# Kernel optimization log

Hardware: AMD Instinct MI355X
Metric: run time of the kernel (lower is better)

The kernel has to match this reference:

```python
import jax, jax.numpy as jnp
import numpy as np

NUM_GRAPHS = 16
NODES_PER = 1024
D = 128
H = 2
KPOS = 20
E = 262144


def _ln(x, g, b):
    mu = jnp.mean(x, axis=-1, keepdims=True)
    var = jnp.mean((x - mu) ** 2, axis=-1, keepdims=True)
    return (x - mu) * jax.lax.rsqrt(var + 1e-5) * g + b


def setup_inputs() -> dict:
    key = jax.random.key(0)
    ks = jax.random.split(key, 12)
    N = NUM_GRAPHS * NODES_PER
    s = 0.02
    return {
        "x": jax.random.normal(ks[0], (N, D), jnp.float32),
        "pos_enc": jax.random.normal(ks[1], (N, KPOS), jnp.float32),
        "pe_w": jax.random.normal(ks[2], (D, KPOS), jnp.float32) * s,
        "pe_b": jnp.zeros((D,), jnp.float32),
        "in_w": jax.random.normal(ks[3], (3 * D, D), jnp.float32) * s,
        "in_b": jnp.zeros((3 * D,), jnp.float32),
        "out_w": jax.random.normal(ks[4], (D, D), jnp.float32) * s,
        "out_b": jnp.zeros((D,), jnp.float32),
        "ln1_g": jnp.ones((D,), jnp.float32),
        "ln1_b": jnp.zeros((D,), jnp.float32),
        "ln2_g": jnp.ones((D,), jnp.float32),
        "ln2_b": jnp.zeros((D,), jnp.float32),
        "ff1_w": jax.random.normal(ks[5], (4 * D, D), jnp.float32) * s,
        "ff1_b": jnp.zeros((4 * D,), jnp.float32),
        "ff2_w": jax.random.normal(ks[6], (D, 4 * D), jnp.float32) * s,
        "ff2_b": jnp.zeros((D,), jnp.float32),
        "edge_index": jax.random.randint(ks[7], (2, E), 0, N, dtype=jnp.int32),
        "batch": jnp.repeat(jnp.arange(NUM_GRAPHS, dtype=jnp.int32), NODES_PER),
    }


def reference(x, pos_enc, pe_w, pe_b, in_w, in_b, out_w, out_b,
              ln1_g, ln1_b, ln2_g, ln2_b, ff1_w, ff1_b, ff2_w, ff2_b,
              edge_index, batch):
    # pos_enc Linear + add, then per-graph transformer (graphs equal-sized -> batched)
    h = x + pos_enc @ pe_w.T + pe_b  # (N, D)
    h = h.reshape(NUM_GRAPHS, NODES_PER, D)  # (B, S, D)

    hd = D // H
    qkv = h @ in_w.T + in_b  # (B, S, 3D)
    q, k, v = jnp.split(qkv, 3, axis=-1)

    def heads(t):
        return t.reshape(NUM_GRAPHS, NODES_PER, H, hd).transpose(0, 2, 1, 3)

    q, k, v = heads(q), heads(k), heads(v)  # (B, H, S, hd)
    scores = jnp.einsum('bhqd,bhkd->bhqk', q, k) / jnp.float32(np.sqrt(hd))
    attn = jax.nn.softmax(scores, axis=-1)
    ctx = jnp.einsum('bhqk,bhkd->bhqd', attn, v)
    ctx = ctx.transpose(0, 2, 1, 3).reshape(NUM_GRAPHS, NODES_PER, D)
    sa = ctx @ out_w.T + out_b

    # post-norm (PyTorch TransformerEncoderLayer default, eval mode: no dropout)
    h = _ln(h + sa, ln1_g, ln1_b)
    ff = jax.nn.relu(h @ ff1_w.T + ff1_b) @ ff2_w.T + ff2_b
    h = _ln(h + ff, ln2_g, ln2_b)
    return h.reshape(-1, D)
```

## Files before the change

### kernel.cpp

```cpp
#include <hip/hip_runtime.h>

typedef unsigned short u16;

#define NGRAPH 16
#define SEQ    1024
#define DIM    128
#define NHEAD  2
#define HDIM   64
#define KPOS   20
#define NTOT   (NGRAPH*SEQ)
#define QKVD   (3*DIM)

__device__ __forceinline__ float bf2f(u16 u) {
    return __uint_as_float(((unsigned int)u) << 16);
}
__device__ __forceinline__ u16 f2bf(float f) {
    unsigned int u = __float_as_uint(f);
    u += 0x7fffu + ((u >> 16) & 1u);
    return (u16)(u >> 16);
}

template<int CTRL>
__device__ __forceinline__ float dpp_ror(float x) {
    return __int_as_float(__builtin_amdgcn_update_dpp(
        __float_as_int(x), __float_as_int(x), CTRL, 0xF, 0xF, true));
}
__device__ __forceinline__ float row16_max(float x) {
    x = fmaxf(x, dpp_ror<0x121>(x));
    x = fmaxf(x, dpp_ror<0x122>(x));
    x = fmaxf(x, dpp_ror<0x124>(x));
    x = fmaxf(x, dpp_ror<0x128>(x));
    return x;
}
__device__ __forceinline__ float row16_sum(float x) {
    x += dpp_ror<0x121>(x);
    x += dpp_ror<0x122>(x);
    x += dpp_ror<0x124>(x);
    x += dpp_ror<0x128>(x);
    return x;
}

__device__ __forceinline__ float ld1(const void* p, int fbf, size_t i) {
    return fbf ? bf2f(((const u16*)p)[i]) : ((const float*)p)[i];
}
__device__ __forceinline__ float4 ldw8(const void* W, int fbf, size_t i) {
    if (fbf) return *(const float4*)((const u16*)W + i);
    const float* q = (const float*)W + i;
    float4 a = *(const float4*)q, b = *(const float4*)(q + 4);
    float4 r;
    u16* d = (u16*)&r;
    d[0]=f2bf(a.x); d[1]=f2bf(a.y); d[2]=f2bf(a.z); d[3]=f2bf(a.w);
    d[4]=f2bf(b.x); d[5]=f2bf(b.y); d[6]=f2bf(b.z); d[7]=f2bf(b.w);
    return r;
}

typedef __attribute__((ext_vector_type(8))) short bf16x8;
typedef __attribute__((ext_vector_type(4))) float f32x4;

__device__ __forceinline__ void gload16(const u16* g, u16* l) {
    __builtin_amdgcn_global_load_lds(
        (const __attribute__((address_space(1))) unsigned int*)(g),
        (__attribute__((address_space(3))) unsigned int*)(l), 16, 0, 0);
}
#define VMCNT0() asm volatile("s_waitcnt vmcnt(0)" ::: "memory")

__device__ __forceinline__ int detect_bf16(const u16* x) {
    int ok = 1;
    for (int i = 0; i < 256; i += 2) {
        unsigned e = (x[i] >> 7) & 0xFF;
        if (e < 60u || e > 180u) ok = 0;
    }
    return ok;
}
__global__ void detect_kernel(const u16* __restrict__ x, int* __restrict__ flag) {
    if (threadIdx.x == 0 && blockIdx.x == 0) *flag = detect_bf16(x);
}

__global__ __launch_bounds__(256)
void wconv_kernel(const void* __restrict__ in_w, const void* __restrict__ out_w,
                  const void* __restrict__ ff1_w, const void* __restrict__ ff2_w,
                  const u16* __restrict__ x,
                  u16* __restrict__ wbf, int* __restrict__ flag) {
    __shared__ int fsh;
    if (threadIdx.x == 0) {
        int ok = detect_bf16(x);
        fsh = ok;
        if (blockIdx.x == 0) *flag = ok;
    }
    __syncthreads();
    int fbf = fsh;
    int i8 = (blockIdx.x * 256 + threadIdx.x) * 8;
    const void* src; int off;
    if      (i8 <  49152) { src = in_w;  off = i8; }
    else if (i8 <  65536) { src = out_w; off = i8 - 49152; }
    else if (i8 < 131072) { src = ff1_w; off = i8 - 65536; }
    else                  { src = ff2_w; off = i8 - 131072; }
    *(float4*)&wbf[i8] = ldw8(src, fbf, off);
}

__global__ __launch_bounds__(256)
void pe_kernel(const void* __restrict__ x, const void* __restrict__ pos,
               const void* __restrict__ pe_w, const void* __restrict__ pe_b,
               u16* __restrict__ h0, const int* __restrict__ flag) {
    int fbf = *flag;
    __shared__ float wsh[DIM][KPOS + 1];
    int t = threadIdx.x;
    for (int i = t; i < DIM * KPOS; i += 256)
        wsh[i / KPOS][i % KPOS] = ld1(pe_w, fbf, i);
    __syncthreads();
    int row = blockIdx.x * 2 + (t >> 7), d = t & 127;
    float acc = 0.f;
#pragma unroll
    for (int k = 0; k < KPOS; ++k)
        acc += ld1(pos, fbf, (size_t)row * KPOS + k) * wsh[d][k];
    int rs = fbf ? 128 : 256;
    h0[(size_t)row * rs + d] =
        f2bf(ld1(x, fbf, (size_t)row * DIM + d) + acc + ld1(pe_b, fbf, d));
}

__global__ __launch_bounds__(256)
void qkvpe_kernel(const void* __restrict__ x, const void* __restrict__ pos,
                  const void* __restrict__ pe_w, const void* __restrict__ pe_b,
                  const u16* __restrict__ W, const void* __restrict__ bias,
                  u16* __restrict__ h0, u16* __restrict__ qkv,
                  u16* __restrict__ vt, const int* __restrict__ flag) {
    int fbf = *flag;
    int rs  = fbf ? 128 : 256;
    __shared__ __align__(16) u16 Ash[64][128];
    __shared__ __align__(16) u16 Wsh[2][128][128];
    __shared__ float wsh[DIM][KPOS + 1];
    __shared__ float possh[64][KPOS + 1];
    int t = threadIdx.x;
    int w = t >> 6, lane = t & 63, l16 = lane & 15, quad = lane >> 4;
    int n0 = blockIdx.x * 64;
    int xr = (l16 & 7) << 3;

#pragma unroll
    for (int i = 0; i < 8; ++i) {
        int r = w * 4 + i * 16 + (lane >> 4);
        int s = (lane & 15) ^ (r & 7);
        gload16(&W[(size_t)r * 128 + s * 8], &Wsh[0][w * 4 + i * 16][0]);
    }
    for (int i = t; i < DIM * KPOS; i += 256)
        wsh[i / KPOS][i % KPOS] = ld1(pe_w, fbf, i);
    for (int i = t; i < 64 * KPOS; i += 256)
        possh[i / KPOS][i % KPOS] =
            ld1(pos, fbf, (size_t)(n0 + i / KPOS) * KPOS + i % KPOS);
    asm volatile("s_waitcnt lgkmcnt(0)" ::: "memory");
    __builtin_amdgcn_s_barrier();

#pragma unroll
    for (int u = 0; u < 4; ++u) {
        int gu = t + u * 256;
        int r = gu >> 4, g = gu & 15;
        float4 hv;
        u16* hp = (u16*)&hv;
#pragma unroll
        for (int j = 0; j < 8; ++j) {
            int d = g * 8 + j;
            float a = ld1(x, fbf, (size_t)(n0 + r) * DIM + d) + ld1(pe_b, fbf, d);
#pragma unroll
            for (int k = 0; k < KPOS; ++k) a += possh[r][k] * wsh[d][k];
            hp[j] = f2bf(a);
        }
        *(float4*)&Ash[r][(g ^ (r & 7)) * 8] = hv;
        *(float4*)&h0[(size_t)(n0 + r) * rs + g * 8] = hv;
    }
    asm volatile("s_waitcnt lgkmcnt(0)" ::: "memory");
    __builtin_amdgcn_s_barrier();

#pragma unroll
    for (int m = 0; m < 3; ++m) {
        int m0 = m * 128;
        if (m < 2) {
#pragma unroll
            for (int i = 0; i < 8; ++i) {
                int r = w * 4 + i * 16 + (lane >> 4);
                int s = (lane & 15) ^ (r & 7);
                gload16(&W[(size_t)(m0 + 128 + r) * 128 + s * 8],
                        &Wsh[(m + 1) & 1][w * 4 + i * 16][0]);
            }
            asm volatile("s_waitcnt vmcnt(8)" ::: "memory");
        } else {
            asm volatile("s_waitcnt vmcnt(0)" ::: "memory");
        }
        __builtin_amdgcn_s_barrier();
        f32x4 acc[8] = {};
        __builtin_amdgcn_s_setprio(1);
#pragma unroll
        for (int kk = 0; kk < 4; ++kk) {
            bf16x8 af = *(const bf16x8*)&Ash[w * 16 + l16][(kk * 32 + quad * 8) ^ xr];
#pragma unroll
            for (int s = 0; s < 8; ++s) {
                bf16x8 bf = *(const bf16x8*)&Wsh[m & 1][s * 16 + l16][(kk * 32 + quad * 8) ^ xr];
                acc[s] = __builtin_amdgcn_mfma_f32_16x16x32_bf16(af, bf, acc[s], 0, 0, 0);
            }
        }
        __builtin_amdgcn_s_setprio(0);
        float bb[8];
#pragma unroll
        for (int s = 0; s < 8; ++s) bb[s] = ld1(bias, fbf, m0 + s * 16 + l16);
#pragma unroll
        for (int r = 0; r < 4; ++r) {
            int lr = w * 16 + quad * 4 + r;
            if (m == 2) {
                int n = n0 + lr;
                int bg = n >> 10, nl = n & 1023;
#pragma unroll
                for (int s = 0; s < 8; ++s)
                    vt[((size_t)(bg * 128) + s * 16 + l16) * SEQ + nl] =
                        f2bf(acc[s][r] + bb[s]);
            } else {
#pragma unroll
                for (int s = 0; s < 8; ++s)
                    qkv[(size_t)(n0 + lr) * QKVD + m0 + s * 16 + l16] =
                        f2bf(acc[s][r] + bb[s]);
            }
        }
        if (m < 2) __builtin_amdgcn_s_barrier();
    }
}

__global__ __launch_bounds__(256)
void attnout_kernel(const u16* __restrict__ qkv, const u16* __restrict__ vtp,
                    const u16* __restrict__ Wout, const void* __restrict__ out_b,
                    const void* __restrict__ lng, const void* __restrict__ lnb,
                    u16* __restrict__ h01, const int* __restrict__ flag) {
    int fbf = *flag;
    int rs  = fbf ? 128 : 256;
    __shared__ __align__(16) u16 Qsh[64][72];
    __shared__ __align__(16) u16 Ksh[2][64][64];
    __shared__ __align__(16) u16 Vsh[2][64][64];
    __shared__ u16 Psh[64][72];
    __shared__ __align__(16) u16 CtxSh[64][128];
    __shared__ __align__(16) u16 Wsh[128][128];
    int t    = threadIdx.x;
    int w    = t >> 6;
    int lane = t & 63;
    int l16  = lane & 15;
    int quad = lane >> 4;
    int xr   = (l16 & 7) << 3;
    int L = blockIdx.x;
    int g8 = L & 7; int rest = L >> 3;
    int qt = rest & 15; int b = (rest >> 4) * 8 + g8;
    int n0 = b * SEQ + qt * 64;

#pragma unroll
    for (int i = 0; i < 8; ++i) {
        int r = w * 4 + i * 16 + (lane >> 4);
        int s = (lane & 15) ^ (r & 7);
        gload16(&Wout[(size_t)r * 128 + s * 8], &Wsh[w * 4 + i * 16][0]);
    }

#pragma unroll 1
    for (int h = 0; h < NHEAD; ++h) {
#pragma unroll
        for (int i = 0; i < 2; ++i) {
            int idx = t + i * 256;
            int r = idx >> 3, d8 = (idx & 7) * 8;
            float4 qv = *(const float4*)&qkv[(size_t)(n0 + r) * QKVD + h * HDIM + d8];
            u16* qp = (u16*)&qv;
#pragma unroll
            for (int j = 0; j < 8; ++j) qp[j] = f2bf(bf2f(qp[j]) * 0.125f);
            *(float4*)&Qsh[r][d8] = qv;
        }
        const u16* kbase = qkv + (size_t)b * SEQ * QKVD + DIM + h * HDIM;
        const u16* vbase = vtp + (size_t)((b * 2 + h) * 64) * SEQ;

        auto stageKV = [&](int kt, int bf2) {
#pragma unroll
            for (int i = 0; i < 2; ++i) {
                int r = w * 8 + i * 32 + (lane >> 3);
                int s = (lane & 7) ^ (r & 7);
                gload16(&kbase[(size_t)(kt * 64 + r) * QKVD + s * 8],
                        &Ksh[bf2][w * 8 + i * 32][0]);
            }
#pragma unroll
            for (int i = 0; i < 2; ++i) {
                int r = w * 8 + i * 32 + (lane >> 3);
                int s = (lane & 7) ^ (r & 7);
                gload16(&vbase[(size_t)r * SEQ + kt * 64 + s * 8],
                        &Vsh[bf2][w * 8 + i * 32][0]);
            }
        };

        stageKV(0, 0);
        VMCNT0();
        __syncthreads();
        bf16x8 qa0 = *(const bf16x8*)&Qsh[w * 16 + l16][quad * 8];
        bf16x8 qa1 = *(const bf16x8*)&Qsh[w * 16 + l16][32 + quad * 8];

        f32x4 o[4] = {};
        float mrow[4] = {-1e30f, -1e30f, -1e30f, -1e30f};
        float lrow[4] = {};

#pragma unroll 1
        for (int kt = 0; kt < SEQ / 64; ++kt) {
            int cur = kt & 1;
            if (kt + 1 < SEQ / 64) stageKV(kt + 1, cur ^ 1);

            float sc[4][4];
            __builtin_amdgcn_s_setprio(1);
#pragma unroll
            for (int c = 0; c < 4; ++c) {
                bf16x8 kb0 = *(const bf16x8*)&Ksh[cur][c * 16 + l16][(quad * 8) ^ xr];
                bf16x8 kb1 = *(const bf16x8*)&Ksh[cur][c * 16 + l16][(32 + quad * 8) ^ xr];
                f32x4 s = {};
                s = __builtin_amdgcn_mfma_f32_16x16x32_bf16(qa0, kb0, s, 0, 0, 0);
                s = __builtin_amdgcn_mfma_f32_16x16x32_bf16(qa1, kb1, s, 0, 0, 0);
#pragma unroll
                for (int r = 0; r < 4; ++r) sc[c][r] = s[r];
            }
            __builtin_amdgcn_s_setprio(0);
            float alpha[4];
#pragma unroll
            for (int r = 0; r < 4; ++r) {
                float mx = fmaxf(fmaxf(sc[0][r], sc[1][r]), fmaxf(sc[2][r], sc[3][r]));
                mx = row16_max(mx);
                float mnew = fmaxf(mrow[r], mx);
                alpha[r] = __expf(mrow[r] - mnew);
                mrow[r] = mnew;
                float sum = 0.f;
#pragma unroll
                for (int c = 0; c < 4; ++c) {
                    float p = __expf(sc[c][r] - mnew);
                    sc[c][r] = p;
                    sum += p;
                }
                sum = row16_sum(sum);
                lrow[r] = lrow[r] * alpha[r] + sum;
            }
#pragma unroll
            for (int c = 0; c < 4; ++c)
#pragma unroll
                for (int r = 0; r < 4; ++r)
                    Psh[w * 16 + quad * 4 + r][c * 16 + l16] = f2bf(sc[c][r]);
#pragma unroll
            for (int dt = 0; dt < 4; ++dt)
#pragma unroll
                for (int r = 0; r < 4; ++r) o[dt][r] *= alpha[r];
            bf16x8 pa0 = *(const bf16x8*)&Psh[w * 16 + l16][quad * 8];
            bf16x8 pa1 = *(const bf16x8*)&Psh[w * 16 + l16][32 + quad * 8];
            __builtin_amdgcn_s_setprio(1);
#pragma unroll
            for (int dt = 0; dt < 4; ++dt) {
                bf16x8 vb0 = *(const bf16x8*)&Vsh[cur][dt * 16 + l16][(quad * 8) ^ xr];
                bf16x8 vb1 = *(const bf16x8*)&Vsh[cur][dt * 16 + l16][(32 + quad * 8) ^ xr];
                o[dt] = __builtin_amdgcn_mfma_f32_16x16x32_bf16(pa0, vb0, o[dt], 0, 0, 0);
                o[dt] = __builtin_amdgcn_mfma_f32_16x16x32_bf16(pa1, vb1, o[dt], 0, 0, 0);
            }
            __builtin_amdgcn_s_setprio(0);
            if (kt + 1 < SEQ / 64) {
                VMCNT0();
                __syncthreads();
            }
        }
#pragma unroll
        for (int r = 0; r < 4; ++r) {
            float inv = 1.f / lrow[r];
            int lr = w * 16 + quad * 4 + r;
#pragma unroll
            for (int dt = 0; dt < 4; ++dt) {
                int e = h * HDIM + dt * 16 + l16;
                int g = e >> 3;
                CtxSh[lr][((g ^ (lr & 7)) << 3) + (e & 7)] =
                    f2bf(o[dt][r] * inv);
            }
        }
        __syncthreads();
    }

    VMCNT0();
    f32x4 acc[8] = {};
    __builtin_amdgcn_s_setprio(1);
#pragma unroll
    for (int kk = 0; kk < 4; ++kk) {
        bf16x8 af = *(const bf16x8*)&CtxSh[w * 16 + l16][(kk * 32 + quad * 8) ^ xr];
#pragma unroll
        for (int s = 0; s < 8; ++s) {
            bf16x8 bf = *(const bf16x8*)&Wsh[s * 16 + l16][(kk * 32 + quad * 8) ^ xr];
            acc[s] = __builtin_amdgcn_mfma_f32_16x16x32_bf16(af, bf, acc[s], 0, 0, 0);
        }
    }
    __builtin_amdgcn_s_setprio(0);
    float bb[8], gg[8], be[8];
#pragma unroll
    for (int s = 0; s < 8; ++s) {
        bb[s] = ld1(out_b, fbf, s * 16 + l16);
        gg[s] = ld1(lng, fbf, s * 16 + l16);
        be[s] = ld1(lnb, fbf, s * 16 + l16);
    }
#pragma unroll
    for (int r = 0; r < 4; ++r) {
        int lr = w * 16 + quad * 4 + r;
        size_t rg = (size_t)(n0 + lr);
        float v[8];
#pragma unroll
        for (int s = 0; s < 8; ++s)
            v[s] = acc[s][r] + bb[s] + bf2f(h01[rg * rs + s * 16 + l16]);
        float sm = 0.f, sq = 0.f;
#pragma unroll
        for (int s = 0; s < 8; ++s) { sm += v[s]; sq += v[s] * v[s]; }
        sm = row16_sum(sm);
        sq = row16_sum(sq);
        float mu  = sm * (1.f / DIM);
        float var = fmaxf(sq * (1.f / DIM) - mu * mu, 0.f);
        float rsq = rsqrtf(var + 1e-5f);
#pragma unroll
        for (int s = 0; s < 8; ++s)
            h01[rg * rs + s * 16 + l16] =
                f2bf((v[s] - mu) * rsq * gg[s] + be[s]);
    }
}

__global__ __launch_bounds__(256)
void ffn_kernel(const u16* __restrict__ h1, const u16* __restrict__ W1,
                const u16* __restrict__ W2, const void* __restrict__ b1,
                const void* __restrict__ b2,
                const void* __restrict__ lng, const void* __restrict__ lnb,
                void* __restrict__ outp, const int* __restrict__ flag) {
    int fbf = *flag;
    int rs  = fbf ? 128 : 256;
    __shared__ __align__(16) u16 Ash[64][128];
    __shared__ __align__(16) u16 Wsh[2][128][128];
    __shared__ __align__(16) u16 F1sh[4][64][128];
    int t = threadIdx.x;
    int w = t >> 6, lane = t & 63, l16 = lane & 15, quad = lane >> 4;
    int n0 = blockIdx.x * 64;
    int xr = (l16 & 7) << 3;

#pragma unroll
    for (int i = 0; i < 4; ++i) {
        int r = w * 4 + i * 16 + (lane >> 4);
        int s = (lane & 15) ^ (r & 7);
        gload16(&h1[(size_t)(n0 + r) * rs + s * 8], &Ash[w * 4 + i * 16][0]);
    }
#pragma unroll
    for (int i = 0; i < 8; ++i) {
        int r = w * 4 + i * 16 + (lane >> 4);
        int s = (lane & 15) ^ (r & 7);
        gload16(&W1[(size_t)r * 128 + s * 8], &Wsh[0][w * 4 + i * 16][0]);
    }

#pragma unroll
    for (int m = 0; m < 4; ++m) {
#pragma unroll
        for (int i = 0; i < 8; ++i) {
            int r = w * 4 + i * 16 + (lane >> 4);
            int s = (lane & 15) ^ (r & 7);
            if (m < 3)
                gload16(&W1[(size_t)((m + 1) * 128 + r) * 128 + s * 8],
                        &Wsh[(m + 1) & 1][w * 4 + i * 16][0]);
            else
                gload16(&W2[(size_t)r * 512 + s * 8],
                        &Wsh[0][w * 4 + i * 16][0]);
        }
        asm volatile("s_waitcnt vmcnt(8)" ::: "memory");
        __builtin_amdgcn_s_barrier();
        f32x4 acc[8] = {};
        __builtin_amdgcn_s_setprio(1);
#pragma unroll
        for (int kk = 0; kk < 4; ++kk) {
            bf16x8 af = *(const bf16x8*)&Ash[w * 16 + l16][(kk * 32 + quad * 8) ^ xr];
#pragma unroll
            for (int s = 0; s < 8; ++s) {
                bf16x8 bf = *(const bf16x8*)&Wsh[m & 1][s * 16 + l16][(kk * 32 + quad * 8) ^ xr];
                acc[s] = __builtin_amdgcn_mfma_f32_16x16x32_bf16(af, bf, acc[s], 0, 0, 0);
            }
        }
        __builtin_amdgcn_s_setprio(0);
        float bb[8];
#pragma unroll
        for (int s = 0; s < 8; ++s) bb[s] = ld1(b1, fbf, m * 128 + s * 16 + l16);
#pragma unroll
        for (int r = 0; r < 4; ++r) {
            int lr = w * 16 + quad * 4 + r;
#pragma unroll
            for (int s = 0; s < 8; ++s) {
                int g = s * 2 + (l16 >> 3);
                F1sh[m][lr][((g ^ (lr & 7)) << 3) + (l16 & 7)] =
                    f2bf(fmaxf(acc[s][r] + bb[s], 0.f));
            }
        }
        asm volatile("s_waitcnt lgkmcnt(0)" ::: "memory");
        __builtin_amdgcn_s_barrier();
    }

    f32x4 acc2[8] = {};
#pragma unroll
    for (int c = 0; c < 4; ++c) {
        if (c < 3) {
#pragma unroll
            for (int i = 0; i < 8; ++i) {
                int r = w * 4 + i * 16 + (lane >> 4);
                int s = (lane & 15) ^ (r & 7);
                gload16(&W2[(size_t)r * 512 + (c + 1) * 128 + s * 8],
                        &Wsh[(c + 1) & 1][w * 4 + i * 16][0]);
            }
            asm volatile("s_waitcnt vmcnt(8)" ::: "memory");
        } else {
            asm volatile("s_waitcnt vmcnt(0)" ::: "memory");
        }
        __builtin_amdgcn_s_barrier();
        __builtin_amdgcn_s_setprio(1);
#pragma unroll
        for (int kk = 0; kk < 4; ++kk) {
            bf16x8 af = *(const bf16x8*)&F1sh[c][w * 16 + l16][(kk * 32 + quad * 8) ^ xr];
#pragma unroll
            for (int s = 0; s < 8; ++s) {
                bf16x8 bf = *(const bf16x8*)&Wsh[c & 1][s * 16 + l16][(kk * 32 + quad * 8) ^ xr];
                acc2[s] = __builtin_amdgcn_mfma_f32_16x16x32_bf16(af, bf, acc2[s], 0, 0, 0);
            }
        }
        __builtin_amdgcn_s_setprio(0);
        if (c < 3) __builtin_amdgcn_s_barrier();
    }

    float bb[8], gg[8], be[8];
#pragma unroll
    for (int s = 0; s < 8; ++s) {
        bb[s] = ld1(b2, fbf, s * 16 + l16);
        gg[s] = ld1(lng, fbf, s * 16 + l16);
        be[s] = ld1(lnb, fbf, s * 16 + l16);
    }
#pragma unroll
    for (int r = 0; r < 4; ++r) {
        int lr = w * 16 + quad * 4 + r;
        size_t rg = (size_t)(n0 + lr);
        float v[8];
#pragma unroll
        for (int s = 0; s < 8; ++s) {
            int g = s * 2 + (l16 >> 3);
            float resid = bf2f(Ash[lr][((g ^ (lr & 7)) << 3) + (l16 & 7)]);
            v[s] = acc2[s][r] + bb[s] + resid;
        }
        float sm = 0.f, sq = 0.f;
#pragma unroll
        for (int s = 0; s < 8; ++s) { sm += v[s]; sq += v[s] * v[s]; }
        sm = row16_sum(sm);
        sq = row16_sum(sq);
        float mu  = sm * (1.f / DIM);
        float var = fmaxf(sq * (1.f / DIM) - mu * mu, 0.f);
        float rsq = rsqrtf(var + 1e-5f);
        if (fbf) {
            u16* o = (u16*)outp;
#pragma unroll
            for (int s = 0; s < 8; ++s)
                o[rg * 128 + s * 16 + l16] =
                    f2bf((v[s] - mu) * rsq * gg[s] + be[s]);
        } else {
            float* o = (float*)outp;
#pragma unroll
            for (int s = 0; s < 8; ++s)
                o[rg * 128 + s * 16 + l16] =
                    (v[s] - mu) * rsq * gg[s] + be[s];
        }
    }
}

template<int EPI, int NK>
__global__ __launch_bounds__(256)
void mgemm_kernel(const u16* __restrict__ A, const void* __restrict__ W,
                  int wbf16, const void* __restrict__ bias,
                  const u16* __restrict__ resid,
                  const void* __restrict__ lng, const void* __restrict__ lnb,
                  void* __restrict__ outp, u16* __restrict__ vt,
                  int Mtot, int AstrIn,
                  int arow0, int orow0, const int* __restrict__ flag) {
    const int K = NK * 128;
    int fbf  = *flag;
    int wfmt = wbf16 ? 1 : fbf;
    int rs   = fbf ? 128 : 256;
    int Astr = (AstrIn < 0) ? rs : AstrIn;
    __shared__ u16 Ash[64][136];
    __shared__ u16 Wsh[128][136];
    int t = threadIdx.x;
    int w = t >> 6, lane = t & 63, l16 = lane & 15, quad = lane >> 4;
    int n0 = blockIdx.x * 64;
    int m0 = blockIdx.y * 128;
    f32x4 acc[8] = {};
    float4 aR[4], wR[8];
#pragma unroll
    for (int i = 0; i < 4; ++i) {
        int idx = t + i * 256;
        int row = idx >> 4, k8 = (idx & 15) * 8;
        aR[i] = *(const float4*)&A[(size_t)(arow0 + n0 + row) * Astr + k8];
    }
#pragma unroll
    for (int i = 0; i < 8; ++i) {
        int idx = t + i * 256;
        int row = idx >> 4, k8 = (idx & 15) * 8;
        wR[i] = ldw8(W, wfmt, (size_t)(m0 + row) * K + k8);
    }
#pragma unroll 1
    for (int c = 0; c < NK; ++c) {
#pragma unroll
        for (int i = 0; i < 4; ++i) {
            int idx = t + i * 256;
            *(float4*)&Ash[idx >> 4][(idx & 15) * 8] = aR[i];
        }
#pragma unroll
        for (int i = 0; i < 8; ++i) {
            int idx = t + i * 256;
            *(float4*)&Wsh[idx >> 4][(idx & 15) * 8] = wR[i];
        }
        __syncthreads();
        if (c + 1 < NK) {
            int kc = (c + 1) * 128;
#pragma unroll
            for (int i = 0; i < 4; ++i) {
                int idx = t + i * 256;
                int row = idx >> 4, k8 = (idx & 15) * 8;
                aR[i] = *(const float4*)&A[(size_t)(arow0 + n0 + row) * Astr + kc + k8];
            }
#pragma unroll
            for (int i = 0; i < 8; ++i) {
                int idx = t + i * 256;
                int row = idx >> 4, k8 = (idx & 15) * 8;
                wR[i] = ldw8(W, wfmt, (size_t)(m0 + row) * K + kc + k8);
            }
        }
        __builtin_amdgcn_s_setprio(1);
#pragma unroll
        for (int kk = 0; kk < 4; ++kk) {
            bf16x8 af = *(const bf16x8*)&Ash[w * 16 + l16][kk * 32 + quad * 8];
#pragma unroll
            for (int s = 0; s < 8; ++s) {
                bf16x8 bf = *(const bf16x8*)&Wsh[s * 16 + l16][kk * 32 + quad * 8];
                acc[s] = __builtin_amdgcn_mfma_f32_16x16x32_bf16(af, bf, acc[s], 0, 0, 0);
            }
        }
        __builtin_amdgcn_s_setprio(0);
        if (c + 1 < NK) __syncthreads();
    }
    float bb[8];
#pragma unroll
    for (int s = 0; s < 8; ++s) bb[s] = ld1(bias, fbf, m0 + s * 16 + l16);
    float gg[8], be[8];
    if (EPI >= 2) {
#pragma unroll
        for (int s = 0; s < 8; ++s) {
            gg[s] = ld1(lng, fbf, s * 16 + l16);
            be[s] = ld1(lnb, fbf, s * 16 + l16);
        }
    }
#pragma unroll
    for (int r = 0; r < 4; ++r) {
        int lr = w * 16 + quad * 4 + r;
        float v[8];
#pragma unroll
        for (int s = 0; s < 8; ++s) {
            v[s] = acc[s][r] + bb[s];
            if (EPI == 1) v[s] = fmaxf(v[s], 0.f);
        }
        if (EPI <= 1) {
            u16* o = (u16*)outp;
#pragma unroll
            for (int s = 0; s < 8; ++s)
                o[(size_t)(n0 + lr) * Mtot + m0 + s * 16 + l16] = f2bf(v[s]);
        } else {
            size_t rg = (size_t)(orow0 + n0 + lr);
#pragma unroll
            for (int s = 0; s < 8; ++s)
                v[s] += bf2f(resid[rg * rs + s * 16 + l16]);
            float sm = 0.f, sq = 0.f;
#pragma unroll
            for (int s = 0; s < 8; ++s) { sm += v[s]; sq += v[s] * v[s]; }
            sm = row16_sum(sm);
            sq = row16_sum(sq);
            float mu  = sm * (1.f / DIM);
            float var = fmaxf(sq * (1.f / DIM) - mu * mu, 0.f);
            float rsq = rsqrtf(var + 1e-5f);
            if (EPI == 2) {
                u16* o = (u16*)outp;
#pragma unroll
                for (int s = 0; s < 8; ++s)
                    o[rg * rs + s * 16 + l16] =
                        f2bf((v[s] - mu) * rsq * gg[s] + be[s]);
            } else {
                if (fbf) {
                    u16* o = (u16*)outp;
#pragma unroll
                    for (int s = 0; s < 8; ++s)
                        o[rg * 128 + s * 16 + l16] =
                            f2bf((v[s] - mu) * rsq * gg[s] + be[s]);
                } else {
                    float* o = (float*)outp;
#pragma unroll
                    for (int s = 0; s < 8; ++s)
                        o[rg * 128 + s * 16 + l16] =
                            (v[s] - mu) * rsq * gg[s] + be[s];
                }
            }
        }
    }
}

__global__ __launch_bounds__(256)
void attn_lds_kernel(const u16* __restrict__ qkv, u16* __restrict__ ctx) {
    __shared__ u16 Qsh[64][72];
    __shared__ u16 Ksh[64][72];
    __shared__ u16 VshT[64][72];
    __shared__ u16 Psh[64][72];
    int t    = threadIdx.x;
    int w    = t >> 6;
    int lane = t & 63;
    int l16  = lane & 15;
    int quad = lane >> 4;
    int L = blockIdx.x;
    int qt = L & 15, gh = L >> 4;
    int b = gh >> 1, h = gh & 1;

#pragma unroll
    for (int i = 0; i < 2; ++i) {
        int idx = t + i * 256;
        int r = idx >> 3, d8 = (idx & 7) * 8;
        size_t n = (size_t)b * SEQ + qt * 64 + r;
        float4 qv = *(const float4*)&qkv[n * QKVD + h * HDIM + d8];
        u16* qp = (u16*)&qv;
#pragma unroll
        for (int j = 0; j < 8; ++j) qp[j] = f2bf(bf2f(qp[j]) * 0.125f);
        *(float4*)&Qsh[r][d8] = qv;
    }
    int kr = t >> 3, kd8 = (t & 7) * 8;
    int vr = t & 63, vdb = (t >> 6) * 16;
    float4 kR[2], vR[2];
    {
        size_t nk0 = (size_t)b * SEQ + kr;
        kR[0] = *(const float4*)&qkv[nk0 * QKVD + DIM + h * HDIM + kd8];
        kR[1] = *(const float4*)&qkv[(nk0 + 32) * QKVD + DIM + h * HDIM + kd8];
        size_t nv0 = (size_t)b * SEQ + vr;
        vR[0] = *(const float4*)&qkv[nv0 * QKVD + 2 * DIM + h * HDIM + vdb];
        vR[1] = *(const float4*)&qkv[nv0 * QKVD + 2 * DIM + h * HDIM + vdb + 8];
    }
    __syncthreads();
    bf16x8 qa0 = *(const bf16x8*)&Qsh[w * 16 + l16][quad * 8];
    bf16x8 qa1 = *(const bf16x8*)&Qsh[w * 16 + l16][32 + quad * 8];

    f32x4 o[4] = {};
    float mrow[4] = {-1e30f, -1e30f, -1e30f, -1e30f};
    float lrow[4] = {};

#pragma unroll 1
    for (int kt = 0; kt < SEQ / 64; ++kt) {
        *(float4*)&Ksh[kr][kd8]      = kR[0];
        *(float4*)&Ksh[kr + 32][kd8] = kR[1];
        {
            const u16* pa = (const u16*)&vR[0];
            const u16* pb = (const u16*)&vR[1];
#pragma unroll
            for (int j = 0; j < 8; ++j) VshT[vdb + j][vr] = pa[j];
#pragma unroll
            for (int j = 0; j < 8; ++j) VshT[vdb + 8 + j][vr] = pb[j];
        }
        __syncthreads();
        if (kt + 1 < SEQ / 64) {
            size_t nk0 = (size_t)b * SEQ + (kt + 1) * 64 + kr;
            kR[0] = *(const float4*)&qkv[nk0 * QKVD + DIM + h * HDIM + kd8];
            kR[1] = *(const float4*)&qkv[(nk0 + 32) * QKVD + DIM + h * HDIM + kd8];
            size_t nv0 = (size_t)b * SEQ + (kt + 1) * 64 + vr;
            vR[0] = *(const float4*)&qkv[nv0 * QKVD + 2 * DIM + h * HDIM + vdb];
            vR[1] = *(const float4*)&qkv[nv0 * QKVD + 2 * DIM + h * HDIM + vdb + 8];
        }
        float sc[4][4];
        __builtin_amdgcn_s_setprio(1);
#pragma unroll
        for (int c = 0; c < 4; ++c) {
            bf16x8 kb0 = *(const bf16x8*)&Ksh[c * 16 + l16][quad * 8];
            bf16x8 kb1 = *(const bf16x8*)&Ksh[c * 16 + l16][32 + quad * 8];
            f32x4 s = {};
            s = __builtin_amdgcn_mfma_f32_16x16x32_bf16(qa0, kb0, s, 0, 0, 0);
            s = __builtin_amdgcn_mfma_f32_16x16x32_bf16(qa1, kb1, s, 0, 0, 0);
#pragma unroll
            for (int r = 0; r < 4; ++r) sc[c][r] = s[r];
        }
        __builtin_amdgcn_s_setprio(0);
        float alpha[4];
#pragma unroll
        for (int r = 0; r < 4; ++r) {
            float mx = fmaxf(fmaxf(sc[0][r], sc[1][r]), fmaxf(sc[2][r], sc[3][r]));
            mx = row16_max(mx);
            float mnew = fmaxf(mrow[r], mx);
            alpha[r] = __expf(mrow[r] - mnew);
            mrow[r] = mnew;
            float sum = 0.f;
#pragma unroll
            for (int c = 0; c < 4; ++c) {
                float p = __expf(sc[c][r] - mnew);
                sc[c][r] = p;
                sum += p;
            }
            sum = row16_sum(sum);
            lrow[r] = lrow[r] * alpha[r] + sum;
        }
#pragma unroll
        for (int c = 0; c < 4; ++c)
#pragma unroll
            for (int r = 0; r < 4; ++r)
                Psh[w * 16 + quad * 4 + r][c * 16 + l16] = f2bf(sc[c][r]);
#pragma unroll
        for (int dt = 0; dt < 4; ++dt)
#pragma unroll
            for (int r = 0; r < 4; ++r) o[dt][r] *= alpha[r];
        bf16x8 pa0 = *(const bf16x8*)&Psh[w * 16 + l16][quad * 8];
        bf16x8 pa1 = *(const bf16x8*)&Psh[w * 16 + l16][32 + quad * 8];
        __builtin_amdgcn_s_setprio(1);
#pragma unroll
        for (int dt = 0; dt < 4; ++dt) {
            bf16x8 vb0 = *(const bf16x8*)&VshT[dt * 16 + l16][quad * 8];
            bf16x8 vb1 = *(const bf16x8*)&VshT[dt * 16 + l16][32 + quad * 8];
            o[dt] = __builtin_amdgcn_mfma_f32_16x16x32_bf16(pa0, vb0, o[dt], 0, 0, 0);
            o[dt] = __builtin_amdgcn_mfma_f32_16x16x32_bf16(pa1, vb1, o[dt], 0, 0, 0);
        }
        __builtin_amdgcn_s_setprio(0);
        __syncthreads();
    }
#pragma unroll
    for (int r = 0; r < 4; ++r) {
        float inv = 1.f / lrow[r];
        size_t n = (size_t)b * SEQ + qt * 64 + w * 16 + quad * 4 + r;
#pragma unroll
        for (int dt = 0; dt < 4; ++dt)
            ctx[n * DIM + h * HDIM + dt * 16 + l16] = f2bf(o[dt][r] * inv);
    }
}

extern "C" void kernel_launch(void* const* d_in, const int* in_sizes, int n_in,
                              void* d_out, int out_size, void* d_ws, size_t ws_size,
                              hipStream_t stream) {
    const void* x     = d_in[0];
    const void* pos   = d_in[1];
    const void* pe_w  = d_in[2];
    const void* pe_b  = d_in[3];
    const void* in_w  = d_in[4];
    const void* in_b  = d_in[5];
    const void* out_w = d_in[6];
    const void* out_b = d_in[7];
    const void* ln1_g = d_in[8];
    const void* ln1_b = d_in[9];
    const void* ln2_g = d_in[10];
    const void* ln2_b = d_in[11];
    const void* ff1_w = d_in[12];
    const void* ff1_b = d_in[13];
    const void* ff2_w = d_in[14];
    const void* ff2_b = d_in[15];

    char* wsb  = (char*)d_ws;
    int*  flag = (int*)(wsb + ((ws_size - 4) & ~(size_t)3));
    u16*  h01  = (u16*)d_out;
    const size_t MB = 1024 * 1024;

    if (ws_size >= 21 * MB) {
        u16* qkv = (u16*)wsb;
        u16* vt  = (u16*)(wsb + 16 * MB);
        u16* wbf = (u16*)(wsb + 20 * MB);
        u16* wb_in  = wbf;
        u16* wb_out = wbf + 49152;
        u16* wb_ff1 = wbf + 65536;
        u16* wb_ff2 = wbf + 131072;

        wconv_kernel<<<96, 256, 0, stream>>>(in_w, out_w, ff1_w, ff2_w,
                                             (const u16*)x, wbf, flag);
        qkvpe_kernel<<<NTOT / 64, 256, 0, stream>>>(
            x, pos, pe_w, pe_b, wb_in, in_b, h01, qkv, vt, flag);
        attnout_kernel<<<NTOT / 64, 256, 0, stream>>>(
            qkv, vt, wb_out, out_b, ln1_g, ln1_b, h01, flag);
        ffn_kernel<<<NTOT / 64, 256, 0, stream>>>(
            h01, wb_ff1, wb_ff2, ff1_b, ff2_b, ln2_g, ln2_b, d_out, flag);
    } else {
        u16* qkv_g = (u16*)wsb;
        u16* ctx_g = (u16*)(wsb + 768 * 1024);
        u16* f1_g  = (u16*)wsb;
        detect_kernel<<<1, 1, 0, stream>>>((const u16*)x, flag);
        pe_kernel<<<NTOT / 2, 256, 0, stream>>>(x, pos, pe_w, pe_b, h01, flag);
        for (int g = 0; g < NGRAPH; ++g) {
            int row0 = g * SEQ;
            mgemm_kernel<0,1><<<dim3(SEQ / 64, 3), 256, 0, stream>>>(
                h01, in_w, 0, in_b, nullptr, nullptr, nullptr, qkv_g, nullptr,
                QKVD, -1, row0, 0, flag);
            attn_lds_kernel<<<NHEAD * 16, 256, 0, stream>>>(qkv_g, ctx_g);
            mgemm_kernel<2,1><<<dim3(SEQ / 64, 1), 256, 0, stream>>>(
                ctx_g, out_w, 0, out_b, h01, ln1_g, ln1_b, h01, nullptr,
                DIM, DIM, 0, row0, flag);
        }
        for (int g = 0; g < NGRAPH; ++g) {
            int row0 = g * SEQ;
            mgemm_kernel<1,1><<<dim3(SEQ / 64, 4), 256, 0, stream>>>(
                h01, ff1_w, 0, ff1_b, nullptr, nullptr, nullptr, f1_g, nullptr,
                4 * DIM, -1, row0, 0, flag);
            mgemm_kernel<3,4><<<dim3(SEQ / 64, 1), 256, 0, stream>>>(
                f1_g, ff2_w, 0, ff2_b, h01, ln2_g, ln2_b, d_out, nullptr,
                DIM, 4 * DIM, 0, row0, flag);
        }
    }
}
```

Before: 192.8 us.

## Split attention per head across blocks and fuse out-proj+LN1 into FFN kernel

The attention kernel now processes one head per block, which doubles the grid to 512 blocks and removes the serial two-head loop. It writes the context to a global workspace buffer instead of doing the output projection in place. The output projection, residual and first LayerNorm move into the FFN kernel, which reuses F1 shared memory for the context and Wout tiles and keeps the normalized row in LDS for FF1. This trades more parallelism and higher occupancy in attention (it no longer allocates the CtxSh/Wsh LDS) for an extra global round trip of the context.

```diff
diff --git a/kernel.cpp b/kernel.cpp
--- a/kernel.cpp
+++ b/kernel.cpp
@@ -222,18 +222,12 @@
 }
 
 __global__ __launch_bounds__(256)
-void attnout_kernel(const u16* __restrict__ qkv, const u16* __restrict__ vtp,
-                    const u16* __restrict__ Wout, const void* __restrict__ out_b,
-                    const void* __restrict__ lng, const void* __restrict__ lnb,
-                    u16* __restrict__ h01, const int* __restrict__ flag) {
-    int fbf = *flag;
-    int rs  = fbf ? 128 : 256;
+void attn2_kernel(const u16* __restrict__ qkv, const u16* __restrict__ vtp,
+                  u16* __restrict__ ctx) {
     __shared__ __align__(16) u16 Qsh[64][72];
     __shared__ __align__(16) u16 Ksh[2][64][64];
     __shared__ __align__(16) u16 Vsh[2][64][64];
     __shared__ u16 Psh[64][72];
-    __shared__ __align__(16) u16 CtxSh[64][128];
-    __shared__ __align__(16) u16 Wsh[128][128];
     int t    = threadIdx.x;
     int w    = t >> 6;
     int lane = t & 63;
@@ -241,189 +235,145 @@
     int quad = lane >> 4;
     int xr   = (l16 & 7) << 3;
     int L = blockIdx.x;
-    int g8 = L & 7; int rest = L >> 3;
-    int qt = rest & 15; int b = (rest >> 4) * 8 + g8;
-    int n0 = b * SEQ + qt * 64;
-
-#pragma unroll
-    for (int i = 0; i < 8; ++i) {
-        int r = w * 4 + i * 16 + (lane >> 4);
-        int s = (lane & 15) ^ (r & 7);
-        gload16(&Wout[(size_t)r * 128 + s * 8], &Wsh[w * 4 + i * 16][0]);
-    }
+    int ngh = gridDim.x >> 4;
+    int qt, gh;
+    if (ngh >= 8) {
+        int g8 = L & 7; int rest = L >> 3;
+        qt = rest & 15; gh = (rest >> 4) * 8 + g8;
+    } else {
+        qt = L & 15; gh = L >> 4;
+    }
+    int b = gh >> 1, h = gh & 1;
+
+#pragma unroll
+    for (int i = 0; i < 2; ++i) {
+        int idx = t + i * 256;
+        int r = idx >> 3, d8 = (idx & 7) * 8;
+        size_t n = (size_t)b * SEQ + qt * 64 + r;
+        float4 qv = *(const float4*)&qkv[n * QKVD + h * HDIM + d8];
+        u16* qp = (u16*)&qv;
+#pragma unroll
+        for (int j = 0; j < 8; ++j) qp[j] = f2bf(bf2f(qp[j]) * 0.125f);
+        *(float4*)&Qsh[r][d8] = qv;
+    }
+
+    const u16* kbase = qkv + (size_t)b * SEQ * QKVD + DIM + h * HDIM;
+    const u16* vbase = vtp + (size_t)((b * 2 + h) * 64) * SEQ;
+
+    auto stageKV = [&](int kt, int bf) {
+#pragma unroll
+        for (int i = 0; i < 2; ++i) {
+            int r = w * 8 + i * 32 + (lane >> 3);
+            int s = (lane & 7) ^ (r & 7);
+            gload16(&kbase[(size_t)(kt * 64 + r) * QKVD + s * 8],
+                    &Ksh[bf][w * 8 + i * 32][0]);
+        }
+#pragma unroll
+        for (int i = 0; i < 2; ++i) {
+            int r = w * 8 + i * 32 + (lane >> 3);
+            int s = (lane & 7) ^ (r & 7);
+            gload16(&vbase[(size_t)r * SEQ + kt * 64 + s * 8],
+                    &Vsh[bf][w * 8 + i * 32][0]);
+        }
+    };
+
+    stageKV(0, 0);
+    VMCNT0();
+    __syncthreads();
+    bf16x8 qa0 = *(const bf16x8*)&Qsh[w * 16 + l16][quad * 8];
+    bf16x8 qa1 = *(const bf16x8*)&Qsh[w * 16 + l16][32 + quad * 8];
+
+    f32x4 o[4] = {};
+    float mrow[4] = {-1e30f, -1e30f, -1e30f, -1e30f};
+    float lrow[4] = {};
 
 #pragma unroll 1
-    for (int h = 0; h < NHEAD; ++h) {
-#pragma unroll
-        for (int i = 0; i < 2; ++i) {
-            int idx = t + i * 256;
-            int r = idx >> 3, d8 = (idx & 7) * 8;
-            float4 qv = *(const float4*)&qkv[(size_t)(n0 + r) * QKVD + h * HDIM + d8];
-            u16* qp = (u16*)&qv;
-#pragma unroll
-            for (int j = 0; j < 8; ++j) qp[j] = f2bf(bf2f(qp[j]) * 0.125f);
-            *(float4*)&Qsh[r][d8] = qv;
-        }
-        const u16* kbase = qkv + (size_t)b * SEQ * QKVD + DIM + h * HDIM;
-        const u16* vbase = vtp + (size_t)((b * 2 + h) * 64) * SEQ;
-
-        auto stageKV = [&](int kt, int bf2) {
-#pragma unroll
-            for (int i = 0; i < 2; ++i) {
-                int r = w * 8 + i * 32 + (lane >> 3);
-                int s = (lane & 7) ^ (r & 7);
-                gload16(&kbase[(size_t)(kt * 64 + r) * QKVD + s * 8],
-                        &Ksh[bf2][w * 8 + i * 32][0]);
-            }
-#pragma unroll
-            for (int i = 0; i < 2; ++i) {
-                int r = w * 8 + i * 32 + (lane >> 3);
-                int s = (lane & 7) ^ (r & 7);
-                gload16(&vbase[(size_t)r * SEQ + kt * 64 + s * 8],
-                        &Vsh[bf2][w * 8 + i * 32][0]);
-            }
-        };
-
-        stageKV(0, 0);
-        VMCNT0();
-        __syncthreads();
-        bf16x8 qa0 = *(const bf16x8*)&Qsh[w * 16 + l16][quad * 8];
-        bf16x8 qa1 = *(const bf16x8*)&Qsh[w * 16 + l16][32 + quad * 8];
-
-        f32x4 o[4] = {};
-        float mrow[4] = {-1e30f, -1e30f, -1e30f, -1e30f};
-        float lrow[4] = {};
-
-#pragma unroll 1
-        for (int kt = 0; kt < SEQ / 64; ++kt) {
-            int cur = kt & 1;
-            if (kt + 1 < SEQ / 64) stageKV(kt + 1, cur ^ 1);
-
-            float sc[4][4];
-            __builtin_amdgcn_s_setprio(1);
+    for (int kt = 0; kt < SEQ / 64; ++kt) {
+        int cur = kt & 1;
+        if (kt + 1 < SEQ / 64) stageKV(kt + 1, cur ^ 1);
+
+        float sc[4][4];
+        __builtin_amdgcn_s_setprio(1);
+#pragma unroll
+        for (int c = 0; c < 4; ++c) {
+            bf16x8 kb0 = *(const bf16x8*)&Ksh[cur][c * 16 + l16][(quad * 8) ^ xr];
+            bf16x8 kb1 = *(const bf16x8*)&Ksh[cur][c * 16 + l16][(32 + quad * 8) ^ xr];
+            f32x4 s = {};
+            s = __builtin_amdgcn_mfma_f32_16x16x32_bf16(qa0, kb0, s, 0, 0, 0);
+            s = __builtin_amdgcn_mfma_f32_16x16x32_bf16(qa1, kb1, s, 0, 0, 0);
+#pragma unroll
+            for (int r = 0; r < 4; ++r) sc[c][r] = s[r];
+        }
+        __builtin_amdgcn_s_setprio(0);
+        float alpha[4];
+#pragma unroll
+        for (int r = 0; r < 4; ++r) {
+            float mx = fmaxf(fmaxf(sc[0][r], sc[1][r]), fmaxf(sc[2][r], sc[3][r]));
+            mx = row16_max(mx);
+            float mnew = fmaxf(mrow[r], mx);
+            alpha[r] = __expf(mrow[r] - mnew);
+            mrow[r] = mnew;
+            float sum = 0.f;
 #pragma unroll
             for (int c = 0; c < 4; ++c) {
-                bf16x8 kb0 = *(const bf16x8*)&Ksh[cur][c * 16 + l16][(quad * 8) ^ xr];
-                bf16x8 kb1 = *(const bf16x8*)&Ksh[cur][c * 16 + l16][(32 + quad * 8) ^ xr];
-                f32x4 s = {};
-                s = __builtin_amdgcn_mfma_f32_16x16x32_bf16(qa0, kb0, s, 0, 0, 0);
-                s = __builtin_amdgcn_mfma_f32_16x16x32_bf16(qa1, kb1, s, 0, 0, 0);
-#pragma unroll
-                for (int r = 0; r < 4; ++r) sc[c][r] = s[r];
-            }
-            __builtin_amdgcn_s_setprio(0);
-            float alpha[4];
-#pragma unroll
-            for (int r = 0; r < 4; ++r) {
-                float mx = fmaxf(fmaxf(sc[0][r], sc[1][r]), fmaxf(sc[2][r], sc[3][r]));
-                mx = row16_max(mx);
-                float mnew = fmaxf(mrow[r], mx);
-                alpha[r] = __expf(mrow[r] - mnew);
-                mrow[r] = mnew;
-                float sum = 0.f;
-#pragma unroll
-                for (int c = 0; c < 4; ++c) {
-                    float p = __expf(sc[c][r] - mnew);
-                    sc[c][r] = p;
-                    sum += p;
-                }
-                sum = row16_sum(sum);
-                lrow[r] = lrow[r] * alpha[r] + sum;
-            }
-#pragma unroll
-            for (int c = 0; c < 4; ++c)
-#pragma unroll
-                for (int r = 0; r < 4; ++r)
-                    Psh[w * 16 + quad * 4 + r][c * 16 + l16] = f2bf(sc[c][r]);
-#pragma unroll
-            for (int dt = 0; dt < 4; ++dt)
-#pragma unroll
-                for (int r = 0; r < 4; ++r) o[dt][r] *= alpha[r];
-            bf16x8 pa0 = *(const bf16x8*)&Psh[w * 16 + l16][quad * 8];
-            bf16x8 pa1 = *(const bf16x8*)&Psh[w * 16 + l16][32 + quad * 8];
-            __builtin_amdgcn_s_setprio(1);
-#pragma unroll
-            for (int dt = 0; dt < 4; ++dt) {
-                bf16x8 vb0 = *(const bf16x8*)&Vsh[cur][dt * 16 + l16][(quad * 8) ^ xr];
-                bf16x8 vb1 = *(const bf16x8*)&Vsh[cur][dt * 16 + l16][(32 + quad * 8) ^ xr];
-                o[dt] = __builtin_amdgcn_mfma_f32_16x16x32_bf16(pa0, vb0, o[dt], 0, 0, 0);
-                o[dt] = __builtin_amdgcn_mfma_f32_16x16x32_bf16(pa1, vb1, o[dt], 0, 0, 0);
-            }
-            __builtin_amdgcn_s_setprio(0);
-            if (kt + 1 < SEQ / 64) {
-                VMCNT0();
-                __syncthreads();
-            }
-        }
-#pragma unroll
-        for (int r = 0; r < 4; ++r) {
-            float inv = 1.f / lrow[r];
-            int lr = w * 16 + quad * 4 + r;
-#pragma unroll
-            for (int dt = 0; dt < 4; ++dt) {
-                int e = h * HDIM + dt * 16 + l16;
-                int g = e >> 3;
-                CtxSh[lr][((g ^ (lr & 7)) << 3) + (e & 7)] =
-                    f2bf(o[dt][r] * inv);
-            }
-        }
-        __syncthreads();
-    }
-
-    VMCNT0();
-    f32x4 acc[8] = {};
-    __builtin_amdgcn_s_setprio(1);
-#pragma unroll
-    for (int kk = 0; kk < 4; ++kk) {
-        bf16x8 af = *(const bf16x8*)&CtxSh[w * 16 + l16][(kk * 32 + quad * 8) ^ xr];
-#pragma unroll
-        for (int s = 0; s < 8; ++s) {
-            bf16x8 bf = *(const bf16x8*)&Wsh[s * 16 + l16][(kk * 32 + quad * 8) ^ xr];
-            acc[s] = __builtin_amdgcn_mfma_f32_16x16x32_bf16(af, bf, acc[s], 0, 0, 0);
-        }
-    }
-    __builtin_amdgcn_s_setprio(0);
-    float bb[8], gg[8], be[8];
-#pragma unroll
-    for (int s = 0; s < 8; ++s) {
-        bb[s] = ld1(out_b, fbf, s * 16 + l16);
-        gg[s] = ld1(lng, fbf, s * 16 + l16);
-        be[s] = ld1(lnb, fbf, s * 16 + l16);
+                float p = __expf(sc[c][r] - mnew);
+                sc[c][r] = p;
+                sum += p;
+            }
+            sum = row16_sum(sum);
+            lrow[r] = lrow[r] * alpha[r] + sum;
+        }
+#pragma unroll
+        for (int c = 0; c < 4; ++c)
+#pragma unroll
+            for (int r = 0; r < 4; ++r)
+                Psh[w * 16 + quad * 4 + r][c * 16 + l16] = f2bf(sc[c][r]);
+#pragma unroll
+        for (int dt = 0; dt < 4; ++dt)
+#pragma unroll
+            for (int r = 0; r < 4; ++r) o[dt][r] *= alpha[r];
+        bf16x8 pa0 = *(const bf16x8*)&Psh[w * 16 + l16][quad * 8];
+        bf16x8 pa1 = *(const bf16x8*)&Psh[w * 16 + l16][32 + quad * 8];
+        __builtin_amdgcn_s_setprio(1);
+#pragma unroll
+        for (int dt = 0; dt < 4; ++dt) {
+            bf16x8 vb0 = *(const bf16x8*)&Vsh[cur][dt * 16 + l16][(quad * 8) ^ xr];
+            bf16x8 vb1 = *(const bf16x8*)&Vsh[cur][dt * 16 + l16][(32 + quad * 8) ^ xr];
+            o[dt] = __builtin_amdgcn_mfma_f32_16x16x32_bf16(pa0, vb0, o[dt], 0, 0, 0);
+            o[dt] = __builtin_amdgcn_mfma_f32_16x16x32_bf16(pa1, vb1, o[dt], 0, 0, 0);
+        }
+        __builtin_amdgcn_s_setprio(0);
+        if (kt + 1 < SEQ / 64) {
+            VMCNT0();
+            __syncthreads();
+        }
     }
 #pragma unroll
     for (int r = 0; r < 4; ++r) {
-        int lr = w * 16 + quad * 4 + r;
-        size_t rg = (size_t)(n0 + lr);
-        float v[8];
-#pragma unroll
-        for (int s = 0; s < 8; ++s)
-            v[s] = acc[s][r] + bb[s] + bf2f(h01[rg * rs + s * 16 + l16]);
-        float sm = 0.f, sq = 0.f;
-#pragma unroll
-        for (int s = 0; s < 8; ++s) { sm += v[s]; sq += v[s] * v[s]; }
-        sm = row16_sum(sm);
-        sq = row16_sum(sq);
-        float mu  = sm * (1.f / DIM);
-        float var = fmaxf(sq * (1.f / DIM) - mu * mu, 0.f);
-        float rsq = rsqrtf(var + 1e-5f);
-#pragma unroll
-        for (int s = 0; s < 8; ++s)
-            h01[rg * rs + s * 16 + l16] =
-                f2bf((v[s] - mu) * rsq * gg[s] + be[s]);
+        float inv = 1.f / lrow[r];
+        size_t n = (size_t)b * SEQ + qt * 64 + w * 16 + quad * 4 + r;
+#pragma unroll
+        for (int dt = 0; dt < 4; ++dt)
+            ctx[n * DIM + h * HDIM + dt * 16 + l16] = f2bf(o[dt][r] * inv);
     }
 }
 
 __global__ __launch_bounds__(256)
-void ffn_kernel(const u16* __restrict__ h1, const u16* __restrict__ W1,
-                const u16* __restrict__ W2, const void* __restrict__ b1,
-                const void* __restrict__ b2,
-                const void* __restrict__ lng, const void* __restrict__ lnb,
-                void* __restrict__ outp, const int* __restrict__ flag) {
+void outffn_kernel(const u16* __restrict__ ctx, const u16* __restrict__ Wout,
+                   const void* __restrict__ out_b,
+                   const void* __restrict__ l1g, const void* __restrict__ l1b,
+                   const u16* __restrict__ h0,
+                   const u16* __restrict__ W1, const u16* __restrict__ W2,
+                   const void* __restrict__ b1, const void* __restrict__ b2,
+                   const void* __restrict__ l2g, const void* __restrict__ l2b,
+                   void* __restrict__ outp, const int* __restrict__ flag) {
     int fbf = *flag;
     int rs  = fbf ? 128 : 256;
     __shared__ __align__(16) u16 Ash[64][128];
     __shared__ __align__(16) u16 Wsh[2][128][128];
     __shared__ __align__(16) u16 F1sh[4][64][128];
+    u16 (*CtxSh)[128]  = (u16(*)[128])&F1sh[0][0][0];
+    u16 (*WoutSh)[128] = (u16(*)[128])&F1sh[2][0][0];
     int t = threadIdx.x;
     int w = t >> 6, lane = t & 63, l16 = lane & 15, quad = lane >> 4;
     int n0 = blockIdx.x * 64;
@@ -433,13 +383,69 @@
     for (int i = 0; i < 4; ++i) {
         int r = w * 4 + i * 16 + (lane >> 4);
         int s = (lane & 15) ^ (r & 7);
-        gload16(&h1[(size_t)(n0 + r) * rs + s * 8], &Ash[w * 4 + i * 16][0]);
+        gload16(&ctx[(size_t)(n0 + r) * DIM + s * 8], &CtxSh[w * 4 + i * 16][0]);
+    }
+#pragma unroll
+    for (int i = 0; i < 8; ++i) {
+        int r = w * 4 + i * 16 + (lane >> 4);
+        int s = (lane & 15) ^ (r & 7);
+        gload16(&Wout[(size_t)r * 128 + s * 8], &WoutSh[w * 4 + i * 16][0]);
     }
 #pragma unroll
     for (int i = 0; i < 8; ++i) {
         int r = w * 4 + i * 16 + (lane >> 4);
         int s = (lane & 15) ^ (r & 7);
         gload16(&W1[(size_t)r * 128 + s * 8], &Wsh[0][w * 4 + i * 16][0]);
+    }
+    asm volatile("s_waitcnt vmcnt(8)" ::: "memory");
+    __builtin_amdgcn_s_barrier();
+
+    {
+        f32x4 acc[8] = {};
+        __builtin_amdgcn_s_setprio(1);
+#pragma unroll
+        for (int kk = 0; kk < 4; ++kk) {
+            bf16x8 af = *(const bf16x8*)&CtxSh[w * 16 + l16][(kk * 32 + quad * 8) ^ xr];
+#pragma unroll
+            for (int s = 0; s < 8; ++s) {
+                bf16x8 bf = *(const bf16x8*)&WoutSh[s * 16 + l16][(kk * 32 + quad * 8) ^ xr];
+                acc[s] = __builtin_amdgcn_mfma_f32_16x16x32_bf16(af, bf, acc[s], 0, 0, 0);
+            }
+        }
+        __builtin_amdgcn_s_setprio(0);
+        float bb[8], gg[8], be[8];
+#pragma unroll
+        for (int s = 0; s < 8; ++s) {
+            bb[s] = ld1(out_b, fbf, s * 16 + l16);
+            gg[s] = ld1(l1g, fbf, s * 16 + l16);
+            be[s] = ld1(l1b, fbf, s * 16 + l16);
+        }
+#pragma unroll
+        for (int r = 0; r < 4; ++r) {
+            int lr = w * 16 + quad * 4 + r;
+            size_t rg = (size_t)(n0 + lr);
+            float v[8];
+#pragma unroll
+            for (int s = 0; s < 8; ++s)
+                v[s] = acc[s][r] + bb[s] + bf2f(h0[rg * rs + s * 16 + l16]);
+            float sm = 0.f, sq = 0.f;
+#pragma unroll
+            for (int s = 0; s < 8; ++s) { sm += v[s]; sq += v[s] * v[s]; }
+            sm = row16_sum(sm);
+            sq = row16_sum(sq);
+            float mu  = sm * (1.f / DIM);
+            float var = fmaxf(sq * (1.f / DIM) - mu * mu, 0.f);
+            float rsq = rsqrtf(var + 1e-5f);
+#pragma unroll
+            for (int s = 0; s < 8; ++s) {
+                int e = s * 16 + l16;
+                int g = e >> 3;
+                Ash[lr][((g ^ (lr & 7)) << 3) + (e & 7)] =
+                    f2bf((v[s] - mu) * rsq * gg[s] + be[s]);
+            }
+        }
+        asm volatile("s_waitcnt lgkmcnt(0)" ::: "memory");
+        __builtin_amdgcn_s_barrier();
     }
 
 #pragma unroll
@@ -520,8 +526,8 @@
 #pragma unroll
     for (int s = 0; s < 8; ++s) {
         bb[s] = ld1(b2, fbf, s * 16 + l16);
-        gg[s] = ld1(lng, fbf, s * 16 + l16);
-        be[s] = ld1(lnb, fbf, s * 16 + l16);
+        gg[s] = ld1(l2g, fbf, s * 16 + l16);
+        be[s] = ld1(l2b, fbf, s * 16 + l16);
     }
 #pragma unroll
     for (int r = 0; r < 4; ++r) {
@@ -852,6 +858,7 @@
 
     if (ws_size >= 21 * MB) {
         u16* qkv = (u16*)wsb;
+        u16* ctx = (u16*)(wsb + 12 * MB);
         u16* vt  = (u16*)(wsb + 16 * MB);
         u16* wbf = (u16*)(wsb + 20 * MB);
         u16* wb_in  = wbf;
@@ -863,10 +870,10 @@
                                              (const u16*)x, wbf, flag);
         qkvpe_kernel<<<NTOT / 64, 256, 0, stream>>>(
             x, pos, pe_w, pe_b, wb_in, in_b, h01, qkv, vt, flag);
-        attnout_kernel<<<NTOT / 64, 256, 0, stream>>>(
-            qkv, vt, wb_out, out_b, ln1_g, ln1_b, h01, flag);
-        ffn_kernel<<<NTOT / 64, 256, 0, stream>>>(
-            h01, wb_ff1, wb_ff2, ff1_b, ff2_b, ln2_g, ln2_b, d_out, flag);
+        attn2_kernel<<<NGRAPH * NHEAD * 16, 256, 0, stream>>>(qkv, vt, ctx);
+        outffn_kernel<<<NTOT / 64, 256, 0, stream>>>(
+            ctx, wb_out, out_b, ln1_g, ln1_b, h01,
+            wb_ff1, wb_ff2, ff1_b, ff2_b, ln2_g, ln2_b, d_out, flag);
     } else {
         u16* qkv_g = (u16*)wsb;
         u16* ctx_g = (u16*)(wsb + 768 * 1024);
```

Result: faster. 172.9 us (-10.3%).
